# Performance work log

Hardware: AMD Instinct MI355X
Metric: run time of the kernel (lower is better)

Reference implementation:

```python
import jax, jax.numpy as jnp
import numpy as np

EMBED = 256
HEADS = 8
HEAD_DIM = 32
MLP_DIM = 1024
NEG = -1e9  # large negative in place of -inf so fully-deselected rows don't NaN
LN_EPS = 1e-5


def _layernorm(x, g, b):
    m = jnp.mean(x, axis=-1, keepdims=True)
    v = jnp.mean(jnp.square(x - m), axis=-1, keepdims=True)
    return (x - m) / jnp.sqrt(v + LN_EPS) * g + b


def setup_inputs() -> dict:
    key = jax.random.key(0)
    ks = jax.random.split(key, 16)
    b, s, d = 64, 360, EMBED
    sc = 0.02
    return {
        "x": jax.random.normal(ks[0], (b, s, d), dtype=jnp.float32),
        "attention_mask": jnp.zeros((b, 1, 1, s), dtype=jnp.float32),
        # TokenRouter.weight_predictor: Linear(256, 1)
        "wp_w": jax.random.normal(ks[1], (1, d), dtype=jnp.float32) * sc,
        "wp_b": jnp.zeros((1,), dtype=jnp.float32),
        # TokenRouter.aux_predictor: Linear(256,128) -> SiLU -> Linear(128,2)
        "a1_w": jax.random.normal(ks[2], (d // 2, d), dtype=jnp.float32) * sc,
        "a1_b": jnp.zeros((d // 2,), dtype=jnp.float32),
        "a2_w": jax.random.normal(ks[3], (2, d // 2), dtype=jnp.float32) * sc,
        "a2_b": jnp.zeros((2,), dtype=jnp.float32),
        # transformer block (pre-LN GPT2-style)
        "ln1_g": jnp.ones((d,), dtype=jnp.float32),
        "ln1_b": jnp.zeros((d,), dtype=jnp.float32),
        "wqkv": jax.random.normal(ks[4], (d, 3 * d), dtype=jnp.float32) * sc,
        "bqkv": jnp.zeros((3 * d,), dtype=jnp.float32),
        "wo": jax.random.normal(ks[5], (d, d), dtype=jnp.float32) * sc,
        "bo": jnp.zeros((d,), dtype=jnp.float32),
        "ln2_g": jnp.ones((d,), dtype=jnp.float32),
        "ln2_b": jnp.zeros((d,), dtype=jnp.float32),
        "w1": jax.random.normal(ks[6], (d, MLP_DIM), dtype=jnp.float32) * sc,
        "b1": jnp.zeros((MLP_DIM,), dtype=jnp.float32),
        "w2": jax.random.normal(ks[7], (MLP_DIM, d), dtype=jnp.float32) * sc,
        "b2": jnp.zeros((d,), dtype=jnp.float32),
    }


def reference(x, attention_mask, wp_w, wp_b, a1_w, a1_b, a2_w, a2_b,
              ln1_g, ln1_b, wqkv, bqkv, wo, bo, ln2_g, ln2_b, w1, b1, w2, b2):
    b, s, d = x.shape
    # --- router: per-token scalar weight ---
    weights = (x @ wp_w.T + wp_b).squeeze(-1)  # [b, s]
    # --- aux predictor selects tokens (eval path: argmax over 2 logits) ---
    h = jax.nn.silu(x @ a1_w.T + a1_b)
    aux_logits = h @ a2_w.T + a2_b            # [b, s, 2]
    sel = jnp.argmax(aux_logits, axis=-1).astype(bool)  # [b, s]
    # --- masked transformer block over the selected token subset.
    # Compacting tokens then attending == full-seq attention with deselected
    # keys masked out (LN/MLP/residual are position-wise), so vectorize:
    bias = attention_mask + jnp.where(sel, 0.0, NEG)[:, None, None, :]  # [b,1,1,s]
    hn = _layernorm(x, ln1_g, ln1_b)
    qkv = hn @ wqkv + bqkv
    q, k, v = jnp.split(qkv, 3, axis=-1)
    q = q.reshape(b, s, HEADS, HEAD_DIM)
    k = k.reshape(b, s, HEADS, HEAD_DIM)
    v = v.reshape(b, s, HEADS, HEAD_DIM)
    scores = jnp.einsum("bqhd,bkhd->bhqk", q, k) / np.sqrt(HEAD_DIM).astype(np.float32)
    scores = scores + bias                   # [b, h, s, s]
    attn = jax.nn.softmax(scores, axis=-1)
    ctx = jnp.einsum("bhqk,bkhd->bqhd", attn, v).reshape(b, s, d)
    h1 = x + (ctx @ wo + bo)
    h2n = _layernorm(h1, ln2_g, ln2_b)
    block_out = h1 + (jax.nn.gelu(h2n @ w1 + b1) @ w2 + b2)  # [b, s, d]
    # --- scatter-recombine: selected -> weighted block output, else passthrough
    out = jnp.where(sel[..., None], block_out * weights[..., None], x)
    avg_selected = jnp.sum(sel.astype(x.dtype)) / b
    return out, avg_selected
```

## Files before the change

kernel.cpp:

```cpp
#include <hip/hip_runtime.h>
#include <math.h>
#include <stdint.h>

#define TOKN 23040
#define BSZ 64
#define SEQ 360
#define DIM 256
#define NHD 8
#define HDD 32
#define MLPD 1024
#define NEGV -1e9f

typedef __attribute__((ext_vector_type(8))) short bf16x8;
typedef __attribute__((ext_vector_type(4))) float f32x4;

static __device__ __forceinline__ short f2bs(float f) {
  unsigned u = __builtin_bit_cast(unsigned, f);
  u += 0x7fffu + ((u >> 16) & 1u);
  return (short)(u >> 16);
}
static __device__ __forceinline__ float bf2f(short s) {
  unsigned u = ((unsigned)(unsigned short)s) << 16;
  return __builtin_bit_cast(float, u);
}
static __device__ __forceinline__ unsigned packbf(float a, float b) {
  return (unsigned)(unsigned short)f2bs(a) | ((unsigned)(unsigned short)f2bs(b) << 16);
}
static __device__ __forceinline__ void gl16(const short* g, short* l) {
  __builtin_amdgcn_global_load_lds(
      (const __attribute__((address_space(1))) unsigned int*)g,
      (__attribute__((address_space(3))) unsigned int*)l, 16, 0, 0);
}

__global__ __launch_bounds__(256) void convw_k(
    const float* __restrict__ wqkv, const float* __restrict__ wo,
    const float* __restrict__ w1, const float* __restrict__ w2,
    short* __restrict__ wqkvt, short* __restrict__ wot,
    short* __restrict__ w1t, short* __restrict__ w2t) {
  int id = blockIdx.x * 256 + threadIdx.x;
  if (id < 256 * 768) {
    int k = id / 768, n = id % 768;
    wqkvt[n * 256 + k] = f2bs(wqkv[id]);
  }
  if (id < 256 * 256) {
    int k = id >> 8, n = id & 255;
    wot[n * 256 + k] = f2bs(wo[id]);
  }
  if (id < 256 * 1024) {
    int k = id >> 10, n = id & 1023;
    w1t[n * 256 + k] = f2bs(w1[id]);
  }
  if (id < 1024 * 256) {
    int k = id >> 8, n = id & 255;
    w2t[n * 1024 + k] = f2bs(w2[id]);
  }
}

__global__ __launch_bounds__(256) void ln_router_k(
    const float* __restrict__ in, const float* __restrict__ g,
    const float* __restrict__ b, const float* __restrict__ wpw,
    const float* __restrict__ wpb, short* __restrict__ outn,
    float* __restrict__ wout, float* __restrict__ outx) {
  int tok = blockIdx.x * 4 + (threadIdx.x >> 6);
  int lane = threadIdx.x & 63;
  const float4 xv = *(const float4*)(in + (size_t)tok * DIM + lane * 4);
  *(float4*)(outx + (size_t)tok * DIM + lane * 4) = xv;
  float s = xv.x + xv.y + xv.z + xv.w;
  float s2 = xv.x * xv.x + xv.y * xv.y + xv.z * xv.z + xv.w * xv.w;
#pragma unroll
  for (int o = 1; o < 64; o <<= 1) { s += __shfl_xor(s, o); s2 += __shfl_xor(s2, o); }
  float m = s * (1.f / DIM);
  float var = fmaxf(s2 * (1.f / DIM) - m * m, 0.f);
  float rstd = rsqrtf(var + 1e-5f);
  float4 gv = *(const float4*)(g + lane * 4);
  float4 bv = *(const float4*)(b + lane * 4);
  uint2 pk;
  pk.x = packbf((xv.x - m) * rstd * gv.x + bv.x, (xv.y - m) * rstd * gv.y + bv.y);
  pk.y = packbf((xv.z - m) * rstd * gv.z + bv.z, (xv.w - m) * rstd * gv.w + bv.w);
  *(uint2*)(outn + (size_t)tok * DIM + lane * 4) = pk;
  float4 wv = *(const float4*)(wpw + lane * 4);
  float wd = xv.x * wv.x + xv.y * wv.y + xv.z * wv.z + xv.w * wv.w;
#pragma unroll
  for (int o = 1; o < 64; o <<= 1) wd += __shfl_xor(wd, o);
  if (lane == 0) wout[tok] = wd + wpb[0];
}

__global__ __launch_bounds__(256) void ln_k(
    const short* __restrict__ in, const float* __restrict__ g,
    const float* __restrict__ b, const int* __restrict__ mtotp,
    short* __restrict__ outn) {
  int tok = blockIdx.x * 4 + (threadIdx.x >> 6);
  int lane = threadIdx.x & 63;
  if (tok >= *mtotp) return;
  union { uint2 v; short s[4]; } u;
  u.v = *(const uint2*)(in + (size_t)tok * DIM + lane * 4);
  float x0 = bf2f(u.s[0]), x1 = bf2f(u.s[1]), x2 = bf2f(u.s[2]), x3 = bf2f(u.s[3]);
  float s = x0 + x1 + x2 + x3;
  float s2 = x0 * x0 + x1 * x1 + x2 * x2 + x3 * x3;
#pragma unroll
  for (int o = 1; o < 64; o <<= 1) { s += __shfl_xor(s, o); s2 += __shfl_xor(s2, o); }
  float m = s * (1.f / DIM);
  float var = fmaxf(s2 * (1.f / DIM) - m * m, 0.f);
  float rstd = rsqrtf(var + 1e-5f);
  float4 gv = *(const float4*)(g + lane * 4);
  float4 bv = *(const float4*)(b + lane * 4);
  uint2 pk;
  pk.x = packbf((x0 - m) * rstd * gv.x + bv.x, (x1 - m) * rstd * gv.y + bv.y);
  pk.y = packbf((x2 - m) * rstd * gv.z + bv.z, (x3 - m) * rstd * gv.w + bv.w);
  *(uint2*)(outn + (size_t)tok * DIM + lane * 4) = pk;
}

__global__ __launch_bounds__(256) void router_gemm_k(
    const float* __restrict__ x, const float* __restrict__ a1w,
    const float* __restrict__ a1b, const float* __restrict__ a2w,
    const float* __restrict__ a2b, int* __restrict__ sel) {
  __shared__ __align__(16) float XT[32][36];
  __shared__ __align__(16) float WT[32][128];
  int m0 = blockIdx.x * 32;
  int t = threadIdx.x;
  int tx = t & 31, ty = t >> 5;
  float acc[4][4] = {};
  int r = t >> 3, c = (t & 7) * 4;
  int n2 = t >> 1, c2 = (t & 1) * 16;
  for (int k0 = 0; k0 < 256; k0 += 32) {
    float4 xa = *(const float4*)(x + (size_t)(m0 + r) * 256 + k0 + c);
    XT[c + 0][r] = xa.x; XT[c + 1][r] = xa.y; XT[c + 2][r] = xa.z; XT[c + 3][r] = xa.w;
#pragma unroll
    for (int j = 0; j < 4; j++) {
      float4 wv = *(const float4*)(a1w + (size_t)n2 * 256 + k0 + c2 + j * 4);
      WT[c2 + j * 4 + 0][n2] = wv.x;
      WT[c2 + j * 4 + 1][n2] = wv.y;
      WT[c2 + j * 4 + 2][n2] = wv.z;
      WT[c2 + j * 4 + 3][n2] = wv.w;
    }
    __syncthreads();
#pragma unroll 8
    for (int kk = 0; kk < 32; kk++) {
      float4 wv4 = *(const float4*)&WT[kk][tx * 4];
      float4 xv4 = *(const float4*)&XT[kk][ty * 4];
      float xr[4] = {xv4.x, xv4.y, xv4.z, xv4.w};
      float wr[4] = {wv4.x, wv4.y, wv4.z, wv4.w};
#pragma unroll
      for (int i = 0; i < 4; i++)
#pragma unroll
        for (int j = 0; j < 4; j++) acc[i][j] += xr[i] * wr[j];
    }
    __syncthreads();
  }
  float b1v[4], a20[4], a21[4];
#pragma unroll
  for (int j = 0; j < 4; j++) {
    int dim = tx * 4 + j;
    b1v[j] = a1b[dim];
    a20[j] = a2w[dim];
    a21[j] = a2w[128 + dim];
  }
  float bias0 = a2b[0], bias1 = a2b[1];
#pragma unroll
  for (int i = 0; i < 4; i++) {
    float l0 = 0.f, l1 = 0.f;
#pragma unroll
    for (int j = 0; j < 4; j++) {
      float v = acc[i][j] + b1v[j];
      float h = v / (1.f + expf(-v));
      l0 += h * a20[j];
      l1 += h * a21[j];
    }
#pragma unroll
    for (int o = 1; o < 32; o <<= 1) { l0 += __shfl_xor(l0, o); l1 += __shfl_xor(l1, o); }
    if (tx == 0) sel[m0 + ty * 4 + i] = (l1 + bias1 > l0 + bias0) ? 1 : 0;
  }
}

__global__ __launch_bounds__(512) void scanA_k(const int* __restrict__ sel,
                                               int* __restrict__ idxl,
                                               int* __restrict__ cnt) {
  __shared__ int sc[512];
  int b = blockIdx.x, t = threadIdx.x;
  int flag = (t < SEQ) ? sel[b * SEQ + t] : 0;
  sc[t] = flag;
  __syncthreads();
  int val = flag;
  for (int off = 1; off < 512; off <<= 1) {
    int add = (t >= off) ? sc[t - off] : 0;
    __syncthreads();
    val += add;
    sc[t] = val;
    __syncthreads();
  }
  if (flag) idxl[b * SEQ + (val - 1)] = t;
  if (t == 511) cnt[b] = val;
}

__global__ __launch_bounds__(512) void scanB_k(const int* __restrict__ cnt,
                                               int* __restrict__ startp,
                                               int* __restrict__ mtotp,
                                               int* __restrict__ g_idx,
                                               float* __restrict__ outavg) {
  __shared__ int sc[64];
  __shared__ int mt;
  int t = threadIdx.x;
  if (t < 64) sc[t] = cnt[t];
  __syncthreads();
  if (t == 0) {
    int run = 0;
    for (int b = 0; b < 64; b++) { startp[b] = run; run += sc[b]; }
    *mtotp = run;
    mt = run;
    outavg[0] = (float)run / 64.0f;
  }
  __syncthreads();
  int m = mt;
  for (int i = m + t; i < TOKN; i += 512) g_idx[i] = 0;
}

__global__ __launch_bounds__(512) void scanC_k(const int* __restrict__ idxl,
                                               const int* __restrict__ startp,
                                               const int* __restrict__ cnt,
                                               int* __restrict__ g_idx) {
  int b = blockIdx.x, t = threadIdx.x;
  int c = cnt[b], s0 = startp[b];
  for (int j = t; j < c; j += 512) g_idx[s0 + j] = b * SEQ + idxl[b * SEQ + j];
}

template <int MODE>
__global__ __launch_bounds__(256) void gemm_bt_k(
    const short* __restrict__ A, const short* __restrict__ Bt,
    const float* __restrict__ bias, const float* __restrict__ resf,
    const short* __restrict__ resb, const float* __restrict__ wgt,
    const int* __restrict__ g_idx, const int* __restrict__ mtotp,
    short* __restrict__ outb, float* __restrict__ outf, int Ndim, int Kdim) {
  int Mt = *mtotp;
  int m0 = blockIdx.y * 64;
  if (m0 >= Mt) return;
  __shared__ __align__(16) short As0[64 * 32];
  __shared__ __align__(16) short As1[64 * 32];
  __shared__ __align__(16) short Bs0[64 * 32];
  __shared__ __align__(16) short Bs1[64 * 32];
  int n0 = blockIdx.x * 64;
  int t = threadIdx.x;
  int wave = t >> 6, lane = t & 63;
  int l15 = lane & 15, quad = lane >> 4;
  int wr = (wave >> 1) * 32, wc = (wave & 1) * 32;
  int r0 = t >> 2, c0 = (t & 3) * 8;
  long ar0 = (MODE == 0) ? g_idx[m0 + r0] : (m0 + r0);
  const short* gA = A + ar0 * Kdim + c0;
  const short* gB = Bt + (size_t)(n0 + r0) * Kdim + c0;
  short* lA0 = As0 + wave * 512;
  short* lA1 = As1 + wave * 512;
  short* lB0 = Bs0 + wave * 512;
  short* lB1 = Bs1 + wave * 512;

  f32x4 acc[2][2];
#pragma unroll
  for (int i = 0; i < 2; i++)
#pragma unroll
    for (int j = 0; j < 2; j++)
#pragma unroll
      for (int r = 0; r < 4; r++) acc[i][j][r] = 0.f;

  for (int k0 = 0; k0 < Kdim; k0 += 64) {
    gl16(gA + k0, lA0);
    gl16(gA + k0 + 32, lA1);
    gl16(gB + k0, lB0);
    gl16(gB + k0 + 32, lB1);
    __syncthreads();
    bf16x8 a0[2], a1[2], b0[2], b1[2];
#pragma unroll
    for (int i = 0; i < 2; i++) {
      a0[i] = *(const bf16x8*)&As0[(wr + i * 16 + l15) * 32 + quad * 8];
      a1[i] = *(const bf16x8*)&As1[(wr + i * 16 + l15) * 32 + quad * 8];
      b0[i] = *(const bf16x8*)&Bs0[(wc + i * 16 + l15) * 32 + quad * 8];
      b1[i] = *(const bf16x8*)&Bs1[(wc + i * 16 + l15) * 32 + quad * 8];
    }
#pragma unroll
    for (int i = 0; i < 2; i++)
#pragma unroll
      for (int j = 0; j < 2; j++) {
        acc[i][j] = __builtin_amdgcn_mfma_f32_16x16x32_bf16(a0[i], b0[j],
                                                            acc[i][j], 0, 0, 0);
        acc[i][j] = __builtin_amdgcn_mfma_f32_16x16x32_bf16(a1[i], b1[j],
                                                            acc[i][j], 0, 0, 0);
      }
    __syncthreads();
  }

#pragma unroll
  for (int i = 0; i < 2; i++) {
#pragma unroll
    for (int j = 0; j < 2; j++) {
      int col = n0 + wc + j * 16 + l15;
      float bcol = bias[col];
#pragma unroll
      for (int r = 0; r < 4; r++) {
        int row = m0 + wr + i * 16 + quad * 4 + r;
        float v = acc[i][j][r] + bcol;
        size_t idx = (size_t)row * Ndim + col;
        if (MODE == 0) {
          outb[idx] = f2bs(v);
        } else if (MODE == 1) {
          int orig = g_idx[row];
          outb[idx] = f2bs(v + resf[(size_t)orig * 256 + col]);
        } else if (MODE == 2) {
          float u = 0.7978845608028654f * (v + 0.044715f * v * v * v);
          float e = __expf(2.f * u);
          float th = 1.f - 2.f / (e + 1.f);
          outb[idx] = f2bs(0.5f * v * (1.f + th));
        } else {
          if (row < Mt) {
            int orig = g_idx[row];
            float o = (v + bf2f(resb[idx])) * wgt[orig];
            outf[(size_t)orig * 256 + col] = o;
          }
        }
      }
    }
  }
}

__global__ __launch_bounds__(256) void attn_k(
    const short* __restrict__ qkv, const float* __restrict__ amask,
    const int* __restrict__ g_idx, const int* __restrict__ startp,
    const int* __restrict__ cntp, short* __restrict__ ctx) {
  __shared__ __align__(16) short VF[2 * 12 * 64 * 8];
  __shared__ __align__(16) float ls[384];
  int bh = blockIdx.x >> 1, qhalf = blockIdx.x & 1;
  int bb = bh >> 3, h = bh & 7;
  int t = threadIdx.x;
  int start = startp[bb], cnt = cntp[bb];
  size_t base = (size_t)start * 768;
  for (int i = t; i < 1536; i += 256) {
    int k = i >> 2, cg = (i & 3) * 8;
    union { int4 v; short s[8]; } u;
    if (k < cnt) {
      u.v = *(const int4*)(qkv + base + (size_t)k * 768 + 512 + h * 32 + cg);
    } else {
      u.v = make_int4(0, 0, 0, 0);
    }
    int c = k >> 5, qd = (k >> 3) & 3, j = k & 7;
#pragma unroll
    for (int jj = 0; jj < 8; jj++) {
      int d = cg + jj;
      VF[((((d >> 4) * 12 + c) * 64) + qd * 16 + (d & 15)) * 8 + j] = u.s[jj];
    }
  }
  for (int i = t; i < 384; i += 256)
    ls[i] = (i < cnt) ? amask[g_idx[start + i]] : 0.f;
  __syncthreads();

  int wave = t >> 6, lane = t & 63;
  int ql = lane & 15, quad = lane >> 4;
  int addr0 = (((quad & 1) * 2) * 16 + ql) * 4;
  int addr1 = addr0 + 64;
  bool hiq = quad >= 2;
  int nt = (cnt + 15) >> 4;
  int nc = (cnt + 31) >> 5;

  for (int qt = qhalf + 2 * wave; qt < nt; qt += 8) {
    int q0 = qt * 16, qrow = q0 + ql;
    bf16x8 qf;
#pragma unroll
    for (int j = 0; j < 8; j++) qf[j] = 0;
    if (qrow < cnt)
      qf = *(const bf16x8*)(qkv + base + (size_t)qrow * 768 + h * 32 + quad * 8);

    f32x4 o0, o1;
#pragma unroll
    for (int r = 0; r < 4; r++) { o0[r] = 0.f; o1[r] = 0.f; }
    float lsum = 0.f;

    for (int c = 0; c < nc; c++) {
      int keyA = c * 32 + ql;
      int keyB = keyA + 16;
      bf16x8 kfA, kfB;
#pragma unroll
      for (int j = 0; j < 8; j++) { kfA[j] = 0; kfB[j] = 0; }
      if (keyA < cnt)
        kfA = *(const bf16x8*)(qkv + base + (size_t)keyA * 768 + 256 + h * 32 + quad * 8);
      if (keyB < cnt)
        kfB = *(const bf16x8*)(qkv + base + (size_t)keyB * 768 + 256 + h * 32 + quad * 8);
      f32x4 sa, sb;
#pragma unroll
      for (int r = 0; r < 4; r++) { sa[r] = 0.f; sb[r] = 0.f; }
      sa = __builtin_amdgcn_mfma_f32_16x16x32_bf16(kfA, qf, sa, 0, 0, 0);
      sb = __builtin_amdgcn_mfma_f32_16x16x32_bf16(kfB, qf, sb, 0, 0, 0);
      int kbase = c * 32 + quad * 4;
      float4 la = *(const float4*)&ls[kbase];
      float4 lb = *(const float4*)&ls[kbase + 16];
      float ea0 = (kbase + 0 < cnt) ? __expf(sa[0] * 0.17677669529663687f + la.x) : 0.f;
      float ea1 = (kbase + 1 < cnt) ? __expf(sa[1] * 0.17677669529663687f + la.y) : 0.f;
      float ea2 = (kbase + 2 < cnt) ? __expf(sa[2] * 0.17677669529663687f + la.z) : 0.f;
      float ea3 = (kbase + 3 < cnt) ? __expf(sa[3] * 0.17677669529663687f + la.w) : 0.f;
      float eb0 = (kbase + 16 < cnt) ? __expf(sb[0] * 0.17677669529663687f + lb.x) : 0.f;
      float eb1 = (kbase + 17 < cnt) ? __expf(sb[1] * 0.17677669529663687f + lb.y) : 0.f;
      float eb2 = (kbase + 18 < cnt) ? __expf(sb[2] * 0.17677669529663687f + lb.z) : 0.f;
      float eb3 = (kbase + 19 < cnt) ? __expf(sb[3] * 0.17677669529663687f + lb.w) : 0.f;
      lsum += (ea0 + ea1) + (ea2 + ea3) + (eb0 + eb1) + (eb2 + eb3);
      unsigned pA0 = packbf(ea0, ea1), pA1 = packbf(ea2, ea3);
      unsigned pB0 = packbf(eb0, eb1), pB1 = packbf(eb2, eb3);
      int s00 = __builtin_amdgcn_ds_bpermute(addr0, (int)pA0);
      int s10 = __builtin_amdgcn_ds_bpermute(addr0, (int)pB0);
      int s01 = __builtin_amdgcn_ds_bpermute(addr0, (int)pA1);
      int s11 = __builtin_amdgcn_ds_bpermute(addr0, (int)pB1);
      int s02 = __builtin_amdgcn_ds_bpermute(addr1, (int)pA0);
      int s12 = __builtin_amdgcn_ds_bpermute(addr1, (int)pB0);
      int s03 = __builtin_amdgcn_ds_bpermute(addr1, (int)pA1);
      int s13 = __builtin_amdgcn_ds_bpermute(addr1, (int)pB1);
      union { int i[4]; bf16x8 v; } pf;
      pf.i[0] = hiq ? s10 : s00;
      pf.i[1] = hiq ? s11 : s01;
      pf.i[2] = hiq ? s12 : s02;
      pf.i[3] = hiq ? s13 : s03;
      bf16x8 v0 = *(const bf16x8*)&VF[(c * 64 + lane) * 8];
      bf16x8 v1 = *(const bf16x8*)&VF[((12 + c) * 64 + lane) * 8];
      o0 = __builtin_amdgcn_mfma_f32_16x16x32_bf16(v0, pf.v, o0, 0, 0, 0);
      o1 = __builtin_amdgcn_mfma_f32_16x16x32_bf16(v1, pf.v, o1, 0, 0, 0);
    }
    lsum += __shfl_xor(lsum, 16);
    lsum += __shfl_xor(lsum, 32);
    float inv = 1.f / lsum;

    if (qrow < cnt) {
      size_t cb = ((size_t)(start + qrow)) * 256 + h * 32;
      uint2 w0, w1;
      w0.x = packbf(o0[0] * inv, o0[1] * inv);
      w0.y = packbf(o0[2] * inv, o0[3] * inv);
      w1.x = packbf(o1[0] * inv, o1[1] * inv);
      w1.y = packbf(o1[2] * inv, o1[3] * inv);
      *(uint2*)(ctx + cb + quad * 4) = w0;
      *(uint2*)(ctx + cb + 16 + quad * 4) = w1;
    }
  }
}

extern "C" void kernel_launch(void* const* d_in, const int* in_sizes, int n_in,
                              void* d_out, int out_size, void* d_ws,
                              size_t ws_size, hipStream_t stream) {
  const float* x = (const float*)d_in[0];
  const float* amask = (const float*)d_in[1];
  const float* wp_w = (const float*)d_in[2];
  const float* wp_b = (const float*)d_in[3];
  const float* a1_w = (const float*)d_in[4];
  const float* a1_b = (const float*)d_in[5];
  const float* a2_w = (const float*)d_in[6];
  const float* a2_b = (const float*)d_in[7];
  const float* ln1_g = (const float*)d_in[8];
  const float* ln1_b = (const float*)d_in[9];
  const float* wqkv = (const float*)d_in[10];
  const float* bqkv = (const float*)d_in[11];
  const float* wo = (const float*)d_in[12];
  const float* bo = (const float*)d_in[13];
  const float* ln2_g = (const float*)d_in[14];
  const float* ln2_b = (const float*)d_in[15];
  const float* w1 = (const float*)d_in[16];
  const float* b1 = (const float*)d_in[17];
  const float* w2 = (const float*)d_in[18];
  const float* b2 = (const float*)d_in[19];
  float* out = (float*)d_out;

  uint8_t* p = (uint8_t*)d_ws;
  float* weightsv = (float*)p; p += (size_t)TOKN * 4;
  int* selv = (int*)p;         p += (size_t)TOKN * 4;
  int* idxlv = (int*)p;        p += (size_t)TOKN * 4;
  int* gidxv = (int*)p;        p += (size_t)TOKN * 4;
  int* cntv = (int*)p;         p += 64 * 4;
  int* startv = (int*)p;       p += 64 * 4;
  int* mtotv = (int*)p;        p += 64 * 4;
  short* wqkvt = (short*)p;    p += (size_t)768 * 256 * 2;
  short* wot = (short*)p;      p += (size_t)256 * 256 * 2;
  short* w1t = (short*)p;      p += (size_t)1024 * 256 * 2;
  short* w2t = (short*)p;      p += (size_t)256 * 1024 * 2;
  short* h1bv = (short*)p;     p += (size_t)TOKN * 256 * 2;
  short* h2nv = (short*)p;     p += (size_t)TOKN * 256 * 2;
  short* ctxv = (short*)p;     p += (size_t)TOKN * 256 * 2;
  uint8_t* R = p;
  short* xnv = (short*)R;
  short* qkvv = (short*)(R + (size_t)TOKN * 256 * 2);
  short* actv = (short*)R;

  convw_k<<<dim3(1024), dim3(256), 0, stream>>>(wqkv, wo, w1, w2, wqkvt, wot, w1t, w2t);
  ln_router_k<<<dim3(TOKN / 4), dim3(256), 0, stream>>>(x, ln1_g, ln1_b, wp_w, wp_b,
                                                        xnv, weightsv, out);
  router_gemm_k<<<dim3(720), dim3(256), 0, stream>>>(x, a1_w, a1_b, a2_w, a2_b, selv);
  scanA_k<<<dim3(64), dim3(512), 0, stream>>>(selv, idxlv, cntv);
  scanB_k<<<dim3(1), dim3(512), 0, stream>>>(cntv, startv, mtotv, gidxv,
                                             out + (size_t)TOKN * 256);
  scanC_k<<<dim3(64), dim3(512), 0, stream>>>(idxlv, startv, cntv, gidxv);
  gemm_bt_k<0><<<dim3(12, 360), dim3(256), 0, stream>>>(
      xnv, wqkvt, bqkv, nullptr, nullptr, nullptr, gidxv, mtotv, qkvv, nullptr,
      768, 256);
  attn_k<<<dim3(1024), dim3(256), 0, stream>>>(qkvv, amask, gidxv, startv, cntv, ctxv);
  gemm_bt_k<1><<<dim3(4, 360), dim3(256), 0, stream>>>(
      ctxv, wot, bo, x, nullptr, nullptr, gidxv, mtotv, h1bv, nullptr, 256, 256);
  ln_k<<<dim3(TOKN / 4), dim3(256), 0, stream>>>(h1bv, ln2_g, ln2_b, mtotv, h2nv);
  gemm_bt_k<2><<<dim3(16, 360), dim3(256), 0, stream>>>(
      h2nv, w1t, b1, nullptr, nullptr, nullptr, gidxv, mtotv, actv, nullptr,
      1024, 256);
  gemm_bt_k<3><<<dim3(4, 360), dim3(256), 0, stream>>>(
      actv, w2t, b2, nullptr, h1bv, weightsv, gidxv, mtotv, nullptr, out, 256, 1024);
}
```

Before: 245.8 us.

## Use 128x128 GEMM tiles with 32x32x16 MFMA and padded LDS staging

Replaces the 64x64-tile GEMM with a 128x128 tile per block. Each wave computes a 64x64 sub-tile using 32x32x16 bf16 MFMA instructions. Operands are loaded from global memory into registers and then stored into padded (stride 72) shared memory, replacing direct global-to-LDS loads. This aims to raise arithmetic intensity and cut redundant operand loads, at the cost of more registers, lower occupancy, and coarser tiles that may waste work or leave CUs idle at the end of the M dimension.

```diff
diff --git a/kernel.cpp b/kernel.cpp
--- a/kernel.cpp
+++ b/kernel.cpp
@@ -13,6 +13,7 @@
 
 typedef __attribute__((ext_vector_type(8))) short bf16x8;
 typedef __attribute__((ext_vector_type(4))) float f32x4;
+typedef __attribute__((ext_vector_type(16))) float f32x16;
 
 static __device__ __forceinline__ short f2bs(float f) {
   unsigned u = __builtin_bit_cast(unsigned, f);
@@ -25,11 +26,6 @@
 }
 static __device__ __forceinline__ unsigned packbf(float a, float b) {
   return (unsigned)(unsigned short)f2bs(a) | ((unsigned)(unsigned short)f2bs(b) << 16);
-}
-static __device__ __forceinline__ void gl16(const short* g, short* l) {
-  __builtin_amdgcn_global_load_lds(
-      (const __attribute__((address_space(1))) unsigned int*)g,
-      (__attribute__((address_space(3))) unsigned int*)l, 16, 0, 0);
 }
 
 __global__ __launch_bounds__(256) void convw_k(
@@ -224,76 +220,84 @@
 }
 
 template <int MODE>
-__global__ __launch_bounds__(256) void gemm_bt_k(
+__global__ __launch_bounds__(256) void gemm32_k(
     const short* __restrict__ A, const short* __restrict__ Bt,
     const float* __restrict__ bias, const float* __restrict__ resf,
     const short* __restrict__ resb, const float* __restrict__ wgt,
     const int* __restrict__ g_idx, const int* __restrict__ mtotp,
     short* __restrict__ outb, float* __restrict__ outf, int Ndim, int Kdim) {
   int Mt = *mtotp;
-  int m0 = blockIdx.y * 64;
+  int m0 = blockIdx.y * 128;
   if (m0 >= Mt) return;
-  __shared__ __align__(16) short As0[64 * 32];
-  __shared__ __align__(16) short As1[64 * 32];
-  __shared__ __align__(16) short Bs0[64 * 32];
-  __shared__ __align__(16) short Bs1[64 * 32];
-  int n0 = blockIdx.x * 64;
+  __shared__ __align__(16) short As[128 * 72];
+  __shared__ __align__(16) short Bs[128 * 72];
+  int n0 = blockIdx.x * 128;
   int t = threadIdx.x;
   int wave = t >> 6, lane = t & 63;
-  int l15 = lane & 15, quad = lane >> 4;
-  int wr = (wave >> 1) * 32, wc = (wave & 1) * 32;
-  int r0 = t >> 2, c0 = (t & 3) * 8;
-  long ar0 = (MODE == 0) ? g_idx[m0 + r0] : (m0 + r0);
-  const short* gA = A + ar0 * Kdim + c0;
-  const short* gB = Bt + (size_t)(n0 + r0) * Kdim + c0;
-  short* lA0 = As0 + wave * 512;
-  short* lA1 = As1 + wave * 512;
-  short* lB0 = Bs0 + wave * 512;
-  short* lB1 = Bs1 + wave * 512;
-
-  f32x4 acc[2][2];
+  int l31 = lane & 31, hi = lane >> 5;
+  int wrm = (wave >> 1) * 64, wcn = (wave & 1) * 64;
+  int scg = (t & 7) * 8;
+  const short* gA[4];
+  const short* gB[4];
+  int srow[4];
+#pragma unroll
+  for (int q = 0; q < 4; q++) {
+    int r = q * 32 + (t >> 3);
+    srow[q] = r;
+    long ar = (MODE == 0) ? g_idx[m0 + r] : (m0 + r);
+    gA[q] = A + ar * Kdim + scg;
+    gB[q] = Bt + (size_t)(n0 + r) * Kdim + scg;
+  }
+
+  f32x16 acc[2][2];
 #pragma unroll
   for (int i = 0; i < 2; i++)
 #pragma unroll
     for (int j = 0; j < 2; j++)
 #pragma unroll
-      for (int r = 0; r < 4; r++) acc[i][j][r] = 0.f;
+      for (int r = 0; r < 16; r++) acc[i][j][r] = 0.f;
 
   for (int k0 = 0; k0 < Kdim; k0 += 64) {
-    gl16(gA + k0, lA0);
-    gl16(gA + k0 + 32, lA1);
-    gl16(gB + k0, lB0);
-    gl16(gB + k0 + 32, lB1);
+    int4 av[4], bv[4];
+#pragma unroll
+    for (int q = 0; q < 4; q++) {
+      av[q] = *(const int4*)(gA[q] + k0);
+      bv[q] = *(const int4*)(gB[q] + k0);
+    }
     __syncthreads();
-    bf16x8 a0[2], a1[2], b0[2], b1[2];
-#pragma unroll
-    for (int i = 0; i < 2; i++) {
-      a0[i] = *(const bf16x8*)&As0[(wr + i * 16 + l15) * 32 + quad * 8];
-      a1[i] = *(const bf16x8*)&As1[(wr + i * 16 + l15) * 32 + quad * 8];
-      b0[i] = *(const bf16x8*)&Bs0[(wc + i * 16 + l15) * 32 + quad * 8];
-      b1[i] = *(const bf16x8*)&Bs1[(wc + i * 16 + l15) * 32 + quad * 8];
-    }
-#pragma unroll
-    for (int i = 0; i < 2; i++)
-#pragma unroll
-      for (int j = 0; j < 2; j++) {
-        acc[i][j] = __builtin_amdgcn_mfma_f32_16x16x32_bf16(a0[i], b0[j],
-                                                            acc[i][j], 0, 0, 0);
-        acc[i][j] = __builtin_amdgcn_mfma_f32_16x16x32_bf16(a1[i], b1[j],
-                                                            acc[i][j], 0, 0, 0);
-      }
+#pragma unroll
+    for (int q = 0; q < 4; q++) {
+      *(int4*)&As[srow[q] * 72 + scg] = av[q];
+      *(int4*)&Bs[srow[q] * 72 + scg] = bv[q];
+    }
     __syncthreads();
+#pragma unroll
+    for (int s = 0; s < 4; s++) {
+      bf16x8 af[2], bfr[2];
+#pragma unroll
+      for (int i = 0; i < 2; i++)
+        af[i] = *(const bf16x8*)&As[(wrm + i * 32 + l31) * 72 + s * 16 + hi * 8];
+#pragma unroll
+      for (int j = 0; j < 2; j++)
+        bfr[j] = *(const bf16x8*)&Bs[(wcn + j * 32 + l31) * 72 + s * 16 + hi * 8];
+#pragma unroll
+      for (int i = 0; i < 2; i++)
+#pragma unroll
+        for (int j = 0; j < 2; j++)
+          acc[i][j] = __builtin_amdgcn_mfma_f32_32x32x16_bf16(af[i], bfr[j],
+                                                              acc[i][j], 0, 0, 0);
+    }
   }
 
 #pragma unroll
   for (int i = 0; i < 2; i++) {
 #pragma unroll
     for (int j = 0; j < 2; j++) {
-      int col = n0 + wc + j * 16 + l15;
+      int col = n0 + wcn + j * 32 + l31;
       float bcol = bias[col];
 #pragma unroll
-      for (int r = 0; r < 4; r++) {
-        int row = m0 + wr + i * 16 + quad * 4 + r;
+      for (int r = 0; r < 16; r++) {
+        int row = m0 + wrm + i * 32 + (r & 3) + 8 * (r >> 2) + 4 * hi;
         float v = acc[i][j][r] + bcol;
         size_t idx = (size_t)row * Ndim + col;
         if (MODE == 0) {
@@ -486,16 +490,16 @@
   scanB_k<<<dim3(1), dim3(512), 0, stream>>>(cntv, startv, mtotv, gidxv,
                                              out + (size_t)TOKN * 256);
   scanC_k<<<dim3(64), dim3(512), 0, stream>>>(idxlv, startv, cntv, gidxv);
-  gemm_bt_k<0><<<dim3(12, 360), dim3(256), 0, stream>>>(
+  gemm32_k<0><<<dim3(6, 180), dim3(256), 0, stream>>>(
       xnv, wqkvt, bqkv, nullptr, nullptr, nullptr, gidxv, mtotv, qkvv, nullptr,
       768, 256);
   attn_k<<<dim3(1024), dim3(256), 0, stream>>>(qkvv, amask, gidxv, startv, cntv, ctxv);
-  gemm_bt_k<1><<<dim3(4, 360), dim3(256), 0, stream>>>(
+  gemm32_k<1><<<dim3(2, 180), dim3(256), 0, stream>>>(
       ctxv, wot, bo, x, nullptr, nullptr, gidxv, mtotv, h1bv, nullptr, 256, 256);
   ln_k<<<dim3(TOKN / 4), dim3(256), 0, stream>>>(h1bv, ln2_g, ln2_b, mtotv, h2nv);
-  gemm_bt_k<2><<<dim3(16, 360), dim3(256), 0, stream>>>(
+  gemm32_k<2><<<dim3(8, 180), dim3(256), 0, stream>>>(
       h2nv, w1t, b1, nullptr, nullptr, nullptr, gidxv, mtotv, actv, nullptr,
       1024, 256);
-  gemm_bt_k<3><<<dim3(4, 360), dim3(256), 0, stream>>>(
+  gemm32_k<3><<<dim3(2, 180), dim3(256), 0, stream>>>(
       actv, w2t, b2, nullptr, h1bv, weightsv, gidxv, mtotv, nullptr, out, 256, 1024);
 }
```

Result: slower. 334.1 us (+35.9%).
